# Optimization experiments

Measured on AMD Instinct MI355X. Metric: run time of the kernel, lower is better.

## Reference

```python
import jax, jax.numpy as jnp
import numpy as np

CODEBOOK_SLOTS = 1024
CODEBOOK_DIM = 256
TEMPERATURE = 0.5
BS, W = 32, 2048


def setup_inputs() -> dict:
    key = jax.random.key(0)
    k1, k2, k3 = jax.random.split(key, 3)
    z_e = jax.random.normal(k1, (BS, CODEBOOK_DIM, W), dtype=jnp.float32)
    codebook = jax.random.normal(k2, (CODEBOOK_SLOTS, CODEBOOK_DIM), dtype=jnp.float32)
    gumbel = jax.random.gumbel(k3, (BS * W, CODEBOOK_SLOTS), dtype=jnp.float32)
    return {"z_e": z_e, "codebook": codebook, "gumbel": gumbel}


def reference(z_e, codebook, gumbel):
    bs, feat_dim, w = z_e.shape
    slots = codebook.shape[0]
    log_slots_const = jnp.float32(np.log(slots))
    # (bs, feat_dim, w) -> (bs*w, feat_dim)
    z_flat = jnp.transpose(z_e, (0, 2, 1)).reshape(bs * w, feat_dim)
    # squared-distance matrix: ||z||^2 + ||c||^2 - 2 z.c  -> (bs*w, slots)
    cb_sqr = jnp.sum(codebook ** 2, axis=1)                 # (slots,)
    z_sqr = jnp.sum(z_flat ** 2, axis=1, keepdims=True)     # (bs*w, 1)
    distances = cb_sqr[None, :] + z_sqr - 2.0 * (z_flat @ codebook.T)
    logits = -distances
    # RelaxedOneHotCategorical.rsample: softmax((logits + gumbel)/tau)
    soft_onehot = jax.nn.softmax((logits + gumbel) / TEMPERATURE, axis=1)
    hard_indices = jnp.argmax(soft_onehot, axis=1).reshape(bs, w)
    # weighted codebook lookup -> (bs, feat_dim, w)
    z_q = (soft_onehot @ codebook).reshape(bs, w, feat_dim)
    z_q = jnp.transpose(z_q, (0, 2, 1))
    # dist.probs = softmax(logits)
    probs = jax.nn.softmax(logits, axis=1)
    kl = (probs * (jnp.log(probs + 1e-9) + log_slots_const))
    kl = kl.reshape(bs, w, slots).sum(axis=(1, 2)).mean()
    commit_loss = (probs * distances).reshape(bs, w, slots).sum(axis=(1, 2)).mean()
    return z_q, hard_indices, kl, commit_loss
```

## Files before the change

### kernel.cpp

```cpp
#include <hip/hip_runtime.h>

#define BSZ 32
#define DIMD 256
#define WW 2048
#define SLOTS 1024
#define NROWS (BSZ*WW)
#define LOG_SLOTS 6.931471805599453f
#define THR 4.0f

#define ZQ_N (BSZ*DIMD*WW)
#define IDX_OFF ZQ_N
#define KL_OFF (ZQ_N + NROWS)
#define CM_OFF (KL_OFF + 1)

#define WS_CH   0u
#define WS_CL   524288u
#define WS_PV   1048576u
#define WS_CBSQ 1572864u
#define WS_TOP  1576960u
#define WS_MR   2625536u
#define WS_NORM 11014144u
#define WS_U    11538432u
#define WS_NEED (11538432ull + 134217728ull)

typedef _Float16 half2_t __attribute__((ext_vector_type(2)));
typedef _Float16 half8_t __attribute__((ext_vector_type(8)));
typedef float v4f __attribute__((ext_vector_type(4)));

__device__ __forceinline__ void pmerge(float& m, float& s, float& t, float om, float os, float ot) {
  float M = fmaxf(m, om);
  float ea = __expf(m - M), eb = __expf(om - M);
  s = s * ea + os * eb;
  t = t * ea + ot * eb;
  m = M;
}

__device__ __forceinline__ void top3_merge(float& v1, float& i1, float& v2, float& i2, float& v3,
                                           float ov1, float oi1, float ov2, float oi2, float ov3) {
  bool sw = (ov1 > v1) || (ov1 == v1 && oi1 < i1);
  float a1v = sw ? ov1 : v1, a1i = sw ? oi1 : i1;
  float a2v = sw ? ov2 : v2, a2i = sw ? oi2 : i2;
  float a3v = sw ? ov3 : v3;
  float b1v = sw ? v1 : ov1, b1i = sw ? i1 : oi1;
  float b2v = sw ? v2 : ov2;
  bool a2w = (a2v > b1v) || (a2v == b1v && a2i < b1i);
  v1 = a1v; i1 = a1i;
  v2 = a2w ? a2v : b1v;
  i2 = a2w ? a2i : b1i;
  v3 = a2w ? fmaxf(a3v, b1v) : fmaxf(a2v, b2v);
}

__global__ void k0_zero(float* out) { out[KL_OFF] = 0.f; out[CM_OFF] = 0.f; }

__global__ void k2_pack(const float* __restrict__ cb, _Float16* __restrict__ chs,
                        _Float16* __restrict__ cls, _Float16* __restrict__ pvs,
                        float* __restrict__ cbsq) {
  const int tid = blockIdx.x * 256 + threadIdx.x;
  if (tid < 32768) {
    const int lane = tid & 63;
    {
      const int ks = (tid >> 6) & 7, sblk = tid >> 9;
      const int col = sblk * 16 + (lane & 15);
      const int k0 = ks * 32 + (lane >> 4) * 8;
      half8_t vh, vl;
#pragma unroll
      for (int j = 0; j < 8; ++j) {
        const float v = cb[(size_t)col * DIMD + k0 + j];
        const _Float16 h = (_Float16)v;
        vh[j] = h;
        vl[j] = (_Float16)(v - (float)h);
      }
      *(half8_t*)&chs[(size_t)tid * 8] = vh;
      *(half8_t*)&cls[(size_t)tid * 8] = vl;
    }
    {
      const int idx = tid >> 6;
      const int cf = idx >> 4, dt = idx & 15;
      const int d = dt * 16 + (lane & 15);
      const int s0 = cf * 32 + (lane >> 4) * 8;
      half8_t vp;
#pragma unroll
      for (int j = 0; j < 8; ++j)
        vp[j] = (_Float16)cb[(size_t)(s0 + j) * DIMD + d];
      *(half8_t*)&pvs[(size_t)tid * 8] = vp;
    }
  }
  if (tid < SLOTS) {
    double a = 0.0;
    for (int i = 0; i < DIMD; ++i) { const double v = (double)cb[(size_t)tid * DIMD + i]; a += v * v; }
    cbsq[tid] = (float)a;
  }
}

__device__ __forceinline__ void stage_chunk(const _Float16* __restrict__ chs,
                                            const _Float16* __restrict__ cls,
                                            _Float16* bsh, _Float16* bsl,
                                            int cf, int wv, int lane) {
  const size_t gbase = (size_t)cf * 8192 + wv * 2048 + lane * 8;
#pragma unroll
  for (int i = 0; i < 4; ++i) {
    __builtin_amdgcn_global_load_lds(
        (const __attribute__((address_space(1))) void*)(chs + gbase + i * 512),
        (__attribute__((address_space(3))) void*)(bsh + wv * 2048 + i * 512), 16, 0, 0);
    __builtin_amdgcn_global_load_lds(
        (const __attribute__((address_space(1))) void*)(cls + gbase + i * 512),
        (__attribute__((address_space(3))) void*)(bsl + wv * 2048 + i * 512), 16, 0, 0);
  }
}

__global__ __launch_bounds__(256) __attribute__((amdgpu_waves_per_eu(2)))
void k3_main(const float* __restrict__ z_e, const float* __restrict__ gum,
             const _Float16* __restrict__ chs, const _Float16* __restrict__ cls,
             const float* __restrict__ cbsq, _Float16* __restrict__ ubig,
             float* __restrict__ mrbuf, float2* __restrict__ normbuf,
             float* __restrict__ topw, float* __restrict__ out) {
  __shared__ _Float16 bsh[8192];
  __shared__ _Float16 bsl[8192];
  __shared__ _Float16 ubuf[4][16][44];

  const int t = threadIdx.x, wv = t >> 6, lane = t & 63, l15 = lane & 15, lq = lane >> 4;
  const int r0 = blockIdx.x * 64;
  const int rw = r0 + wv * 16;
  const int rt = blockIdx.x * 4 + wv;
  const int b = r0 >> 11;
  const int w0 = rw & 2047;

  stage_chunk(chs, cls, bsh, bsl, 0, wv, lane);

  const float* zbase = z_e + (size_t)b * DIMD * WW + w0 + l15;
  half8_t ah[8], al[8];
  float zacc = 0.f;
#pragma unroll
  for (int ks = 0; ks < 8; ++ks) {
#pragma unroll
    for (int j = 0; j < 8; ++j) {
      const float v = zbase[(size_t)(ks * 32 + lq * 8 + j) * WW];
      zacc += v * v;
      const _Float16 h = (_Float16)v;
      ah[ks][j] = h;
      al[ks][j] = (_Float16)(v - (float)h);
    }
  }
  zacc += __shfl_xor(zacc, 16);
  zacc += __shfl_xor(zacc, 32);
  float zs[4];
#pragma unroll
  for (int g = 0; g < 4; ++g) zs[g] = __shfl(zacc, lq * 4 + g);

  float m1[4], s1[4], t1[4], v1[4], v2[4], v3[4], i1[4], i2[4], s2[4], mr[4];
#pragma unroll
  for (int g = 0; g < 4; ++g) {
    m1[g] = -1e30f; s1[g] = 0.f; t1[g] = 0.f;
    v1[g] = -1e30f; v2[g] = -1e30f; v3[g] = -1e30f; i1[g] = 0.f; i2[g] = 0.f;
    s2[g] = 0.f; mr[g] = -1e30f;
  }

  const float* gbase = gum + (size_t)rw * SLOTS;
  float gc[8], cbc[2];
#pragma unroll
  for (int c = 0; c < 2; ++c) {
    cbc[c] = cbsq[c * 16 + l15];
#pragma unroll
    for (int g = 0; g < 4; ++g)
      gc[c * 4 + g] = gbase[(size_t)(lq * 4 + g) * SLOTS + c * 16 + l15];
  }

  __syncthreads();

#pragma unroll 1
  for (int cf = 0; cf < 32; ++cf) {
    float gn[8], cbn[2];
    if (cf < 31) {
#pragma unroll
      for (int c = 0; c < 2; ++c) {
        cbn[c] = cbsq[(cf + 1) * 32 + c * 16 + l15];
#pragma unroll
        for (int g = 0; g < 4; ++g)
          gn[c * 4 + g] = gbase[(size_t)(lq * 4 + g) * SLOTS + (cf + 1) * 32 + c * 16 + l15];
      }
    }
    v4f qh[2], ql[2];
    qh[0] = v4f{0.f, 0.f, 0.f, 0.f}; qh[1] = v4f{0.f, 0.f, 0.f, 0.f};
    ql[0] = v4f{0.f, 0.f, 0.f, 0.f}; ql[1] = v4f{0.f, 0.f, 0.f, 0.f};
#pragma unroll
    for (int ks = 0; ks < 8; ++ks) {
      const int o0 = ((0 * 8 + ks) * 64 + lane) * 8;
      const int o1 = ((1 * 8 + ks) * 64 + lane) * 8;
      const half8_t bh0 = *(const half8_t*)&bsh[o0];
      const half8_t bl0 = *(const half8_t*)&bsl[o0];
      const half8_t bh1 = *(const half8_t*)&bsh[o1];
      const half8_t bl1 = *(const half8_t*)&bsl[o1];
      qh[0] = __builtin_amdgcn_mfma_f32_16x16x32_f16(ah[ks], bh0, qh[0], 0, 0, 0);
      ql[0] = __builtin_amdgcn_mfma_f32_16x16x32_f16(al[ks], bh0, ql[0], 0, 0, 0);
      ql[0] = __builtin_amdgcn_mfma_f32_16x16x32_f16(ah[ks], bl0, ql[0], 0, 0, 0);
      qh[1] = __builtin_amdgcn_mfma_f32_16x16x32_f16(ah[ks], bh1, qh[1], 0, 0, 0);
      ql[1] = __builtin_amdgcn_mfma_f32_16x16x32_f16(al[ks], bh1, ql[1], 0, 0, 0);
      ql[1] = __builtin_amdgcn_mfma_f32_16x16x32_f16(ah[ks], bl1, ql[1], 0, 0, 0);
    }
    __syncthreads();
    if (cf < 31) stage_chunk(chs, cls, bsh, bsl, cf + 1, wv, lane);

    float yv[8];
    float cmax[4] = {-1e30f, -1e30f, -1e30f, -1e30f};
#pragma unroll
    for (int c = 0; c < 2; ++c) {
      const int col = cf * 32 + c * 16 + l15;
      const float cq = cbc[c];
      const float fc = (float)col;
#pragma unroll
      for (int g = 0; g < 4; ++g) {
        const float dd = cq + zs[g] - 2.f * (qh[c][g] + ql[c][g]);
        const float lv = -dd;
        if (__builtin_expect(lv > m1[g] + 8.f, 0)) {
          const float f = __expf(m1[g] - lv);
          s1[g] *= f; t1[g] *= f; m1[g] = lv;
        }
        const float e = __expf(lv - m1[g]);
        s1[g] += e;
        t1[g] = __fmaf_rn(e, dd, t1[g]);
        const float y = 2.f * (gc[c * 4 + g] - dd);
        yv[c * 4 + g] = y;
        const bool b1 = (y > v1[g]);
        const bool b2 = (y > v2[g]);
        const bool b3 = (y > v3[g]);
        v3[g] = b2 ? v2[g] : (b3 ? y : v3[g]);
        v2[g] = b1 ? v1[g] : (b2 ? y : v2[g]);
        i2[g] = b1 ? i1[g] : (b2 ? fc : i2[g]);
        v1[g] = b1 ? y : v1[g];
        i1[g] = b1 ? fc : i1[g];
        cmax[g] = fmaxf(cmax[g], y);
      }
    }
#pragma unroll
    for (int mk = 1; mk < 16; mk <<= 1)
#pragma unroll
      for (int g = 0; g < 4; ++g) cmax[g] = fmaxf(cmax[g], __shfl_xor(cmax[g], mk));
#pragma unroll
    for (int g = 0; g < 4; ++g) {
      if (cmax[g] > mr[g] + THR) {
        s2[g] *= __expf(mr[g] - cmax[g]);
        mr[g] = cmax[g];
      }
    }
#pragma unroll
    for (int c = 0; c < 2; ++c)
#pragma unroll
      for (int g = 0; g < 4; ++g) {
        const float u = __expf(yv[c * 4 + g] - mr[g]);
        s2[g] += u;
        ubuf[wv][lq * 4 + g][c * 16 + l15] = (_Float16)u;
      }
    if (l15 == 0) {
#pragma unroll
      for (int g = 0; g < 4; ++g)
        mrbuf[((size_t)rt * 32 + cf) * 16 + lq * 4 + g] = mr[g];
    }
    const half8_t pa = *(const half8_t*)&ubuf[wv][l15][lq * 8];
    *(half8_t*)&ubig[((size_t)rt * 32 + cf) * 512 + l15 * 32 + lq * 8] = pa;
    if (cf < 31) {
#pragma unroll
      for (int i = 0; i < 8; ++i) gc[i] = gn[i];
      cbc[0] = cbn[0]; cbc[1] = cbn[1];
    }
    __syncthreads();
  }

#pragma unroll
  for (int mk = 1; mk < 16; mk <<= 1) {
#pragma unroll
    for (int g = 0; g < 4; ++g) {
      const float om = __shfl_xor(m1[g], mk);
      const float os = __shfl_xor(s1[g], mk);
      const float ot = __shfl_xor(t1[g], mk);
      pmerge(m1[g], s1[g], t1[g], om, os, ot);
      const float ov1 = __shfl_xor(v1[g], mk);
      const float oi1 = __shfl_xor(i1[g], mk);
      const float ov2 = __shfl_xor(v2[g], mk);
      const float oi2 = __shfl_xor(i2[g], mk);
      const float ov3 = __shfl_xor(v3[g], mk);
      top3_merge(v1[g], i1[g], v2[g], i2[g], v3[g], ov1, oi1, ov2, oi2, ov3);
      s2[g] += __shfl_xor(s2[g], mk);
    }
  }
  float klsum = 0.f, cmsum = 0.f;
#pragma unroll
  for (int g = 0; g < 4; ++g) {
    const float commit_row = t1[g] / s1[g];
    const float lse = m1[g] + logf(s1[g]);
    klsum += -commit_row - lse + LOG_SLOTS;
    cmsum += commit_row;
    if (l15 == 0) {
      const int row = rw + lq * 4 + g;
      out[IDX_OFF + row] = i1[g];
      float4 tv; tv.x = v1[g]; tv.y = v2[g]; tv.z = v3[g]; tv.w = i2[g];
      *(float4*)&topw[(size_t)row * 4] = tv;
      normbuf[row] = make_float2(mr[g], 1.f / s2[g]);
    }
  }
  float kw = (l15 == 0) ? klsum : 0.f;
  float cw = (l15 == 0) ? cmsum : 0.f;
#pragma unroll
  for (int mk = 1; mk < 64; mk <<= 1) { kw += __shfl_xor(kw, mk); cw += __shfl_xor(cw, mk); }
  if (lane == 0) {
    atomicAdd(&out[KL_OFF], kw * 0.03125f);
    atomicAdd(&out[CM_OFF], cw * 0.03125f);
  }
}

__global__ __launch_bounds__(256) __attribute__((amdgpu_waves_per_eu(2)))
void k4_pv(const _Float16* __restrict__ ubig, const float* __restrict__ mrbuf,
           const float2* __restrict__ normbuf, const _Float16* __restrict__ pvs,
           float* __restrict__ out) {
  const int t = threadIdx.x, wv = t >> 6, lane = t & 63, l15 = lane & 15, lq = lane >> 4;
  const int rt = blockIdx.x * 4 + wv;
  const int r0 = rt * 16;
  const int b = r0 >> 11, w0 = r0 & 2047;
  const float2 nv = normbuf[r0 + l15];
  const float mrfin = nv.x, inv = nv.y;
  v4f pacc[16];
#pragma unroll
  for (int dt = 0; dt < 16; ++dt) pacc[dt] = v4f{0.f, 0.f, 0.f, 0.f};

  float mrc = mrbuf[(size_t)rt * 32 * 16 + l15];
  half8_t pa0 = *(const half8_t*)&ubig[(size_t)rt * 32 * 512 + l15 * 32 + lq * 8];
#pragma unroll 1
  for (int cf = 0; cf < 32; ++cf) {
    float mrn = 0.f; half8_t pan = pa0;
    if (cf < 31) {
      mrn = mrbuf[((size_t)rt * 32 + cf + 1) * 16 + l15];
      pan = *(const half8_t*)&ubig[((size_t)rt * 32 + cf + 1) * 512 + l15 * 32 + lq * 8];
    }
    const float f = __expf(mrc - mrfin);
    half8_t pa;
#pragma unroll
    for (int j = 0; j < 8; ++j) pa[j] = (_Float16)((float)pa0[j] * f);
#pragma unroll
    for (int dt = 0; dt < 16; ++dt) {
      const half8_t pb = *(const half8_t*)&pvs[((size_t)(cf * 16 + dt) * 64 + lane) * 8];
      pacc[dt] = __builtin_amdgcn_mfma_f32_16x16x32_f16(pb, pa, pacc[dt], 0, 0, 0);
    }
    mrc = mrn; pa0 = pan;
  }
#pragma unroll
  for (int dt = 0; dt < 16; ++dt)
#pragma unroll
    for (int g = 0; g < 4; ++g)
      out[((size_t)b * DIMD + dt * 16 + lq * 4 + g) * WW + w0 + l15] = pacc[dt][g] * inv;
}

__global__ void k5_repair(const float* __restrict__ z_e, const float* __restrict__ cb,
                          const float* __restrict__ gum, const float* __restrict__ topw,
                          float* __restrict__ out) {
  const int wv = threadIdx.x >> 6, lane = threadIdx.x & 63;
#pragma unroll 1
  for (int rr = 0; rr < 64; ++rr) {
    const int r = blockIdx.x * 256 + wv * 64 + rr;
    const float4 tw = *(const float4*)&topw[(size_t)r * 4];
    if (tw.x - tw.y >= 0.02f) continue;
    const int b = r >> 11, w = r & 2047;
    double zd[4]; double zq = 0.0;
#pragma unroll
    for (int i = 0; i < 4; ++i) {
      const float zz = z_e[((size_t)b * DIMD + lane + i * 64) * WW + w];
      zd[i] = (double)zz; zq += zd[i] * zd[i];
    }
#pragma unroll
    for (int mk = 1; mk < 64; mk <<= 1) zq += __shfl_xor(zq, mk);
    const int c1 = (int)out[IDX_OFF + r];
    const int c2 = (int)tw.w;
    const bool full = (tw.x - tw.z < 0.02f);
    double bestv = -1e300; int besti = 0;
    const int nc = full ? SLOTS : 2;
    for (int ci = 0; ci < nc; ++ci) {
      const int s = full ? ci : (ci == 0 ? c1 : c2);
      double dot = 0.0, csq = 0.0;
#pragma unroll
      for (int i = 0; i < 4; ++i) {
        const double cv = (double)cb[(size_t)s * DIMD + lane + i * 64];
        dot += zd[i] * cv; csq += cv * cv;
      }
#pragma unroll
      for (int mk = 1; mk < 64; mk <<= 1) { dot += __shfl_xor(dot, mk); csq += __shfl_xor(csq, mk); }
      const double y = 2.0 * ((double)gum[(size_t)r * SLOTS + s] - (csq + zq - 2.0 * dot));
      if (y > bestv || (y == bestv && s < besti)) { bestv = y; besti = s; }
    }
    if (lane == 0) out[IDX_OFF + r] = (float)besti;
  }
}

extern "C" void kernel_launch(void* const* d_in, const int* in_sizes, int n_in,
                              void* d_out, int out_size, void* d_ws, size_t ws_size,
                              hipStream_t stream) {
  const float* z_e = (const float*)d_in[0];
  const float* cb  = (const float*)d_in[1];
  const float* gum = (const float*)d_in[2];
  float* out = (float*)d_out;
  char* ws = (char*)d_ws;
  if (ws_size < WS_NEED) {
    hipMemsetAsync(d_out, 0, (size_t)out_size * sizeof(float), stream);
    return;
  }
  _Float16* chs = (_Float16*)(ws + WS_CH);
  _Float16* cls = (_Float16*)(ws + WS_CL);
  _Float16* pvs = (_Float16*)(ws + WS_PV);
  float* cbsq = (float*)(ws + WS_CBSQ);
  float* topw = (float*)(ws + WS_TOP);
  float* mrbuf = (float*)(ws + WS_MR);
  float2* normbuf = (float2*)(ws + WS_NORM);
  _Float16* ubig = (_Float16*)(ws + WS_U);
  k0_zero<<<1, 1, 0, stream>>>(out);
  k2_pack<<<128, 256, 0, stream>>>(cb, chs, cls, pvs, cbsq);
  k3_main<<<1024, 256, 0, stream>>>(z_e, gum, chs, cls, cbsq, ubig, mrbuf, normbuf, topw, out);
  k4_pv<<<1024, 256, 0, stream>>>(ubig, mrbuf, normbuf, pvs, out);
  k5_repair<<<256, 256, 0, stream>>>(z_e, cb, gum, topw, out);
}
```

Measured before the change: 459.1 us.

## Pre-pack gumbel noise into MFMA fragment order for coalesced float4 loads

```diff
diff --git a/kernel.cpp b/kernel.cpp
--- a/kernel.cpp
+++ b/kernel.cpp
@@ -21,7 +21,9 @@
 #define WS_MR   2625536u
 #define WS_NORM 11014144u
 #define WS_U    11538432u
-#define WS_NEED (11538432ull + 134217728ull)
+#define WS_GPK  145756160ull
+#define WS_NEED_SMALL 145756160ull
+#define WS_NEED_BIG   (145756160ull + 268435456ull)
 
 typedef _Float16 half2_t __attribute__((ext_vector_type(2)));
 typedef _Float16 half8_t __attribute__((ext_vector_type(8)));
@@ -92,6 +94,46 @@
   }
 }
 
+__global__ __launch_bounds__(256) void k2b_packg(const float* __restrict__ gum,
+                                                 float* __restrict__ gpk) {
+  __shared__ float lds[16 * 1024];
+  const int t = threadIdx.x;
+  const int rt = blockIdx.x;
+  const int r0 = rt * 16;
+  const int lrow = t >> 6;
+  const int lcol = (t & 63) * 4;
+#pragma unroll
+  for (int rr = 0; rr < 4; ++rr) {
+    const int row = rr * 4 + lrow;
+#pragma unroll
+    for (int p = 0; p < 4; ++p) {
+      const int col = lcol + p * 256;
+      const int swz = ((col >> 5) & 7) << 2;
+      *(float4*)&lds[row * 1024 + (col ^ swz)] =
+          *(const float4*)&gum[(size_t)(r0 + row) * SLOTS + col];
+    }
+  }
+  __syncthreads();
+  const int cf = t >> 3;
+  const int sub = t & 7;
+  float* dst = gpk + ((size_t)rt * 32 + cf) * 512 + sub * 64;
+#pragma unroll
+  for (int i = 0; i < 8; ++i) {
+    const int L = sub * 8 + i;
+    const int lq = L >> 4, l15 = L & 15;
+    float4 A, B;
+#pragma unroll
+    for (int j = 0; j < 4; ++j) {
+      const int c0 = cf * 32 + l15;
+      const int c1 = cf * 32 + 16 + l15;
+      ((float*)&A)[j] = lds[(lq * 4 + j) * 1024 + (c0 ^ (((c0 >> 5) & 7) << 2))];
+      ((float*)&B)[j] = lds[(lq * 4 + j) * 1024 + (c1 ^ (((c1 >> 5) & 7) << 2))];
+    }
+    *(float4*)&dst[i * 8] = A;
+    *(float4*)&dst[i * 8 + 4] = B;
+  }
+}
+
 __device__ __forceinline__ void stage_chunk(const _Float16* __restrict__ chs,
                                             const _Float16* __restrict__ cls,
                                             _Float16* bsh, _Float16* bsl,
@@ -108,8 +150,10 @@
   }
 }
 
+template <int GP>
 __global__ __launch_bounds__(256) __attribute__((amdgpu_waves_per_eu(2)))
 void k3_main(const float* __restrict__ z_e, const float* __restrict__ gum,
+             const float* __restrict__ gpk,
              const _Float16* __restrict__ chs, const _Float16* __restrict__ cls,
              const float* __restrict__ cbsq, _Float16* __restrict__ ubig,
              float* __restrict__ mrbuf, float2* __restrict__ normbuf,
@@ -156,14 +200,22 @@
   }
 
   const float* gbase = gum + (size_t)rw * SLOTS;
+  const float4* gpbase = (const float4*)(gpk + (size_t)rt * 32 * 512);
   float gc[8], cbc[2];
-#pragma unroll
-  for (int c = 0; c < 2; ++c) {
-    cbc[c] = cbsq[c * 16 + l15];
-#pragma unroll
-    for (int g = 0; g < 4; ++g)
-      gc[c * 4 + g] = gbase[(size_t)(lq * 4 + g) * SLOTS + c * 16 + l15];
-  }
+  if (GP) {
+    const float4 A = gpbase[lane * 2];
+    const float4 B = gpbase[lane * 2 + 1];
+    gc[0] = A.x; gc[1] = A.y; gc[2] = A.z; gc[3] = A.w;
+    gc[4] = B.x; gc[5] = B.y; gc[6] = B.z; gc[7] = B.w;
+  } else {
+#pragma unroll
+    for (int c = 0; c < 2; ++c)
+#pragma unroll
+      for (int g = 0; g < 4; ++g)
+        gc[c * 4 + g] = gbase[(size_t)(lq * 4 + g) * SLOTS + c * 16 + l15];
+  }
+  cbc[0] = cbsq[l15];
+  cbc[1] = cbsq[16 + l15];
 
   __syncthreads();
 
@@ -171,13 +223,20 @@
   for (int cf = 0; cf < 32; ++cf) {
     float gn[8], cbn[2];
     if (cf < 31) {
-#pragma unroll
-      for (int c = 0; c < 2; ++c) {
-        cbn[c] = cbsq[(cf + 1) * 32 + c * 16 + l15];
-#pragma unroll
-        for (int g = 0; g < 4; ++g)
-          gn[c * 4 + g] = gbase[(size_t)(lq * 4 + g) * SLOTS + (cf + 1) * 32 + c * 16 + l15];
-      }
+      if (GP) {
+        const float4 A = gpbase[(size_t)(cf + 1) * 128 + lane * 2];
+        const float4 B = gpbase[(size_t)(cf + 1) * 128 + lane * 2 + 1];
+        gn[0] = A.x; gn[1] = A.y; gn[2] = A.z; gn[3] = A.w;
+        gn[4] = B.x; gn[5] = B.y; gn[6] = B.z; gn[7] = B.w;
+      } else {
+#pragma unroll
+        for (int c = 0; c < 2; ++c)
+#pragma unroll
+          for (int g = 0; g < 4; ++g)
+            gn[c * 4 + g] = gbase[(size_t)(lq * 4 + g) * SLOTS + (cf + 1) * 32 + c * 16 + l15];
+      }
+      cbn[0] = cbsq[(cf + 1) * 32 + l15];
+      cbn[1] = cbsq[(cf + 1) * 32 + 16 + l15];
     }
     v4f qh[2], ql[2];
     qh[0] = v4f{0.f, 0.f, 0.f, 0.f}; qh[1] = v4f{0.f, 0.f, 0.f, 0.f};
@@ -396,7 +455,7 @@
   const float* gum = (const float*)d_in[2];
   float* out = (float*)d_out;
   char* ws = (char*)d_ws;
-  if (ws_size < WS_NEED) {
+  if (ws_size < WS_NEED_SMALL) {
     hipMemsetAsync(d_out, 0, (size_t)out_size * sizeof(float), stream);
     return;
   }
@@ -408,9 +467,16 @@
   float* mrbuf = (float*)(ws + WS_MR);
   float2* normbuf = (float2*)(ws + WS_NORM);
   _Float16* ubig = (_Float16*)(ws + WS_U);
+  float* gpk = (float*)(ws + WS_GPK);
+  const bool big = (ws_size >= WS_NEED_BIG);
   k0_zero<<<1, 1, 0, stream>>>(out);
   k2_pack<<<128, 256, 0, stream>>>(cb, chs, cls, pvs, cbsq);
-  k3_main<<<1024, 256, 0, stream>>>(z_e, gum, chs, cls, cbsq, ubig, mrbuf, normbuf, topw, out);
+  if (big) {
+    k2b_packg<<<4096, 256, 0, stream>>>(gum, gpk);
+    k3_main<1><<<1024, 256, 0, stream>>>(z_e, gum, gpk, chs, cls, cbsq, ubig, mrbuf, normbuf, topw, out);
+  } else {
+    k3_main<0><<<1024, 256, 0, stream>>>(z_e, gum, gpk, chs, cls, cbsq, ubig, mrbuf, normbuf, topw, out);
+  }
   k4_pv<<<1024, 256, 0, stream>>>(ubig, mrbuf, normbuf, pvs, out);
   k5_repair<<<256, 256, 0, stream>>>(z_e, cb, gum, topw, out);
 }
```

Measured after the change: 624.9 us. 1.36x slower.

## Fuse soft-onehot codebook lookup into main distance kernel with online rescaling

Applied to the files above, without the earlier changes.

```diff
diff --git a/kernel.cpp b/kernel.cpp
--- a/kernel.cpp
+++ b/kernel.cpp
@@ -18,10 +18,7 @@
 #define WS_PV   1048576u
 #define WS_CBSQ 1572864u
 #define WS_TOP  1576960u
-#define WS_MR   2625536u
-#define WS_NORM 11014144u
-#define WS_U    11538432u
-#define WS_NEED (11538432ull + 134217728ull)
+#define WS_NEED (1576960ull + 1048576ull)
 
 typedef _Float16 half2_t __attribute__((ext_vector_type(2)));
 typedef _Float16 half8_t __attribute__((ext_vector_type(8)));
@@ -111,17 +108,16 @@
 __global__ __launch_bounds__(256) __attribute__((amdgpu_waves_per_eu(2)))
 void k3_main(const float* __restrict__ z_e, const float* __restrict__ gum,
              const _Float16* __restrict__ chs, const _Float16* __restrict__ cls,
-             const float* __restrict__ cbsq, _Float16* __restrict__ ubig,
-             float* __restrict__ mrbuf, float2* __restrict__ normbuf,
+             const float* __restrict__ cbsq, const _Float16* __restrict__ pvs,
              float* __restrict__ topw, float* __restrict__ out) {
   __shared__ _Float16 bsh[8192];
   __shared__ _Float16 bsl[8192];
-  __shared__ _Float16 ubuf[4][16][44];
+  __shared__ _Float16 ubuf[2][4][16][44];
+  __shared__ float rowq[2][4][16];
 
   const int t = threadIdx.x, wv = t >> 6, lane = t & 63, l15 = lane & 15, lq = lane >> 4;
   const int r0 = blockIdx.x * 64;
   const int rw = r0 + wv * 16;
-  const int rt = blockIdx.x * 4 + wv;
   const int b = r0 >> 11;
   const int w0 = rw & 2047;
 
@@ -154,6 +150,10 @@
     v1[g] = -1e30f; v2[g] = -1e30f; v3[g] = -1e30f; i1[g] = 0.f; i2[g] = 0.f;
     s2[g] = 0.f; mr[g] = -1e30f;
   }
+  float mcol = -1e30f;
+  v4f pacc[16];
+#pragma unroll
+  for (int dt = 0; dt < 16; ++dt) pacc[dt] = v4f{0.f, 0.f, 0.f, 0.f};
 
   const float* gbase = gum + (size_t)rw * SLOTS;
   float gc[8], cbc[2];
@@ -177,6 +177,24 @@
 #pragma unroll
         for (int g = 0; g < 4; ++g)
           gn[c * 4 + g] = gbase[(size_t)(lq * 4 + g) * SLOTS + (cf + 1) * 32 + c * 16 + l15];
+      }
+    }
+    if (cf > 0) {
+      const int cfm = cf - 1, pp = cfm & 1;
+      const float mprev = rowq[pp][wv][l15];
+      if (mprev != mcol) {
+        const float f = __expf(mcol - mprev);
+#pragma unroll
+        for (int dt = 0; dt < 16; ++dt)
+#pragma unroll
+          for (int g = 0; g < 4; ++g) pacc[dt][g] *= f;
+        mcol = mprev;
+      }
+      const half8_t pa = *(const half8_t*)&ubuf[pp][wv][l15][lq * 8];
+#pragma unroll
+      for (int dt = 0; dt < 16; ++dt) {
+        const half8_t pb = *(const half8_t*)&pvs[((size_t)(cfm * 16 + dt) * 64 + lane) * 8];
+        pacc[dt] = __builtin_amdgcn_mfma_f32_16x16x32_f16(pb, pa, pacc[dt], 0, 0, 0);
       }
     }
     v4f qh[2], ql[2];
@@ -242,27 +260,43 @@
         mr[g] = cmax[g];
       }
     }
+    if (l15 == 0) {
+#pragma unroll
+      for (int g = 0; g < 4; ++g) rowq[cf & 1][wv][lq * 4 + g] = mr[g];
+    }
 #pragma unroll
     for (int c = 0; c < 2; ++c)
 #pragma unroll
       for (int g = 0; g < 4; ++g) {
         const float u = __expf(yv[c * 4 + g] - mr[g]);
         s2[g] += u;
-        ubuf[wv][lq * 4 + g][c * 16 + l15] = (_Float16)u;
-      }
-    if (l15 == 0) {
-#pragma unroll
-      for (int g = 0; g < 4; ++g)
-        mrbuf[((size_t)rt * 32 + cf) * 16 + lq * 4 + g] = mr[g];
-    }
-    const half8_t pa = *(const half8_t*)&ubuf[wv][l15][lq * 8];
-    *(half8_t*)&ubig[((size_t)rt * 32 + cf) * 512 + l15 * 32 + lq * 8] = pa;
+        ubuf[cf & 1][wv][lq * 4 + g][c * 16 + l15] = (_Float16)u;
+      }
     if (cf < 31) {
 #pragma unroll
       for (int i = 0; i < 8; ++i) gc[i] = gn[i];
       cbc[0] = cbn[0]; cbc[1] = cbn[1];
     }
     __syncthreads();
+  }
+
+  {
+    const int pp = 31 & 1;
+    const float mprev = rowq[pp][wv][l15];
+    if (mprev != mcol) {
+      const float f = __expf(mcol - mprev);
+#pragma unroll
+      for (int dt = 0; dt < 16; ++dt)
+#pragma unroll
+        for (int g = 0; g < 4; ++g) pacc[dt][g] *= f;
+      mcol = mprev;
+    }
+    const half8_t pa = *(const half8_t*)&ubuf[pp][wv][l15][lq * 8];
+#pragma unroll
+    for (int dt = 0; dt < 16; ++dt) {
+      const half8_t pb = *(const half8_t*)&pvs[((size_t)(31 * 16 + dt) * 64 + lane) * 8];
+      pacc[dt] = __builtin_amdgcn_mfma_f32_16x16x32_f16(pb, pa, pacc[dt], 0, 0, 0);
+    }
   }
 
 #pragma unroll
@@ -294,9 +328,17 @@
       out[IDX_OFF + row] = i1[g];
       float4 tv; tv.x = v1[g]; tv.y = v2[g]; tv.z = v3[g]; tv.w = i2[g];
       *(float4*)&topw[(size_t)row * 4] = tv;
-      normbuf[row] = make_float2(mr[g], 1.f / s2[g]);
-    }
-  }
+      rowq[0][wv][lq * 4 + g] = 1.f / s2[g];
+    }
+  }
+  __builtin_amdgcn_s_waitcnt(0);
+  const float inv = rowq[0][wv][l15];
+#pragma unroll
+  for (int dt = 0; dt < 16; ++dt)
+#pragma unroll
+    for (int g = 0; g < 4; ++g)
+      out[((size_t)b * DIMD + dt * 16 + lq * 4 + g) * WW + w0 + l15] = pacc[dt][g] * inv;
+
   float kw = (l15 == 0) ? klsum : 0.f;
   float cw = (l15 == 0) ? cmsum : 0.f;
 #pragma unroll
@@ -305,47 +347,6 @@
     atomicAdd(&out[KL_OFF], kw * 0.03125f);
     atomicAdd(&out[CM_OFF], cw * 0.03125f);
   }
-}
-
-__global__ __launch_bounds__(256) __attribute__((amdgpu_waves_per_eu(2)))
-void k4_pv(const _Float16* __restrict__ ubig, const float* __restrict__ mrbuf,
-           const float2* __restrict__ normbuf, const _Float16* __restrict__ pvs,
-           float* __restrict__ out) {
-  const int t = threadIdx.x, wv = t >> 6, lane = t & 63, l15 = lane & 15, lq = lane >> 4;
-  const int rt = blockIdx.x * 4 + wv;
-  const int r0 = rt * 16;
-  const int b = r0 >> 11, w0 = r0 & 2047;
-  const float2 nv = normbuf[r0 + l15];
-  const float mrfin = nv.x, inv = nv.y;
-  v4f pacc[16];
-#pragma unroll
-  for (int dt = 0; dt < 16; ++dt) pacc[dt] = v4f{0.f, 0.f, 0.f, 0.f};
-
-  float mrc = mrbuf[(size_t)rt * 32 * 16 + l15];
-  half8_t pa0 = *(const half8_t*)&ubig[(size_t)rt * 32 * 512 + l15 * 32 + lq * 8];
-#pragma unroll 1
-  for (int cf = 0; cf < 32; ++cf) {
-    float mrn = 0.f; half8_t pan = pa0;
-    if (cf < 31) {
-      mrn = mrbuf[((size_t)rt * 32 + cf + 1) * 16 + l15];
-      pan = *(const half8_t*)&ubig[((size_t)rt * 32 + cf + 1) * 512 + l15 * 32 + lq * 8];
-    }
-    const float f = __expf(mrc - mrfin);
-    half8_t pa;
-#pragma unroll
-    for (int j = 0; j < 8; ++j) pa[j] = (_Float16)((float)pa0[j] * f);
-#pragma unroll
-    for (int dt = 0; dt < 16; ++dt) {
-      const half8_t pb = *(const half8_t*)&pvs[((size_t)(cf * 16 + dt) * 64 + lane) * 8];
-      pacc[dt] = __builtin_amdgcn_mfma_f32_16x16x32_f16(pb, pa, pacc[dt], 0, 0, 0);
-    }
-    mrc = mrn; pa0 = pan;
-  }
-#pragma unroll
-  for (int dt = 0; dt < 16; ++dt)
-#pragma unroll
-    for (int g = 0; g < 4; ++g)
-      out[((size_t)b * DIMD + dt * 16 + lq * 4 + g) * WW + w0 + l15] = pacc[dt][g] * inv;
 }
 
 __global__ void k5_repair(const float* __restrict__ z_e, const float* __restrict__ cb,
@@ -405,12 +406,8 @@
   _Float16* pvs = (_Float16*)(ws + WS_PV);
   float* cbsq = (float*)(ws + WS_CBSQ);
   float* topw = (float*)(ws + WS_TOP);
-  float* mrbuf = (float*)(ws + WS_MR);
-  float2* normbuf = (float2*)(ws + WS_NORM);
-  _Float16* ubig = (_Float16*)(ws + WS_U);
   k0_zero<<<1, 1, 0, stream>>>(out);
   k2_pack<<<128, 256, 0, stream>>>(cb, chs, cls, pvs, cbsq);
-  k3_main<<<1024, 256, 0, stream>>>(z_e, gum, chs, cls, cbsq, ubig, mrbuf, normbuf, topw, out);
-  k4_pv<<<1024, 256, 0, stream>>>(ubig, mrbuf, normbuf, pvs, out);
+  k3_main<<<1024, 256, 0, stream>>>(z_e, gum, chs, cls, cbsq, pvs, topw, out);
   k5_repair<<<256, 256, 0, stream>>>(z_e, cb, gum, topw, out);
 }
```

Result: slower. 604.6 us (+31.7%).
